# Kernel optimization log

Hardware: AMD Instinct MI355X
Metric: run time of the kernel (lower is better)

## Reference

```python
import jax, jax.numpy as jnp
import numpy as np

BATCH, N_FEATURES, D_MODEL = 8192, 8192, 1024


def setup_inputs() -> dict:
    key = jax.random.key(0)
    kx, kw = jax.random.split(key)
    # x: sparse feature activations in the original (COO); dense uniform here.
    x = jax.random.uniform(kx, (BATCH, N_FEATURES), dtype=jnp.float32)
    # Xavier-normal init for W_tr [n_features, d_model].
    std = float(np.sqrt(2.0 / (N_FEATURES + D_MODEL)))
    W_tr = jax.random.normal(kw, (N_FEATURES, D_MODEL), dtype=jnp.float32) * std
    bias = jnp.zeros((N_FEATURES,), dtype=jnp.float32)
    return {"x": x, "W_tr": W_tr, "bias": bias}


def reference(x, W_tr, bias):
    # h = x @ W_tr              : [B, n_features] @ [n_features, d_model] -> [B, d_model]
    # out = relu(h @ W_tr.T + b): [B, d_model] @ [d_model, n_features] -> [B, n_features]
    h = jnp.einsum("bf,fd->bd", x, W_tr)
    return jax.nn.relu(jnp.einsum("bd,fd->bf", h, W_tr) + bias)
```

## Files before the change

### kernel.cpp

```cpp
#include <hip/hip_runtime.h>
#include <hip/hip_bf16.h>
#include <stdint.h>

#define BATCH  8192
#define NFEAT  8192
#define DMODEL 1024

typedef unsigned short u16;
typedef __attribute__((ext_vector_type(8))) short  short8;
typedef __attribute__((ext_vector_type(4))) float  f32x4;

__device__ __forceinline__ u16 f2b(float f) {
    uint32_t u = __float_as_uint(f);
    u += 0x7fffu + ((u >> 16) & 1u);
    return (u16)(u >> 16);
}

__device__ __forceinline__ void gld16(const u16* g, void* l) {
    __builtin_amdgcn_global_load_lds(
        (const __attribute__((address_space(1))) void*)(uintptr_t)g,
        (__attribute__((address_space(3))) void*)(uint32_t)(uintptr_t)l,
        16, 0, 0);
}


__global__ void cvt_x_kernel(const float* __restrict__ x, u16* __restrict__ xb) {
    int i = blockIdx.x * blockDim.x + threadIdx.x;
    const float4* xv = (const float4*)x;
    float4 a = xv[2 * i];
    float4 b = xv[2 * i + 1];
    union { u16 u[8]; uint4 v; } o;
    o.u[0] = f2b(a.x); o.u[1] = f2b(a.y); o.u[2] = f2b(a.z); o.u[3] = f2b(a.w);
    o.u[4] = f2b(b.x); o.u[5] = f2b(b.y); o.u[6] = f2b(b.z); o.u[7] = f2b(b.w);
    ((uint4*)xb)[i] = o.v;
}

__global__ void cvt_w_kernel(const float* __restrict__ W,
                             u16* __restrict__ wb, u16* __restrict__ wt) {
    __shared__ u16 tile[64][65];
    const int f0 = blockIdx.x * 64;
    const int d0 = blockIdx.y * 64;
    const int t  = threadIdx.x;
#pragma unroll
    for (int rep = 0; rep < 16; ++rep) {
        int idx = rep * 256 + t;
        int r = idx >> 6, c = idx & 63;
        float v = W[(size_t)(f0 + r) * DMODEL + d0 + c];
        u16 u = f2b(v);
        tile[r][c] = u;
        wb[(size_t)(f0 + r) * DMODEL + d0 + c] = u;
    }
    __syncthreads();
#pragma unroll
    for (int rep = 0; rep < 16; ++rep) {
        int idx = rep * 256 + t;
        int r = idx >> 6, c = idx & 63;
        wt[(size_t)(d0 + r) * NFEAT + f0 + c] = tile[c][r];
    }
}

#define SYNC_IN()  do { __builtin_amdgcn_s_barrier(); \
                        asm volatile("s_waitcnt lgkmcnt(0)" ::: "memory"); } while (0)
#define SYNC_OUT() do { __builtin_amdgcn_s_setprio(0); __builtin_amdgcn_s_barrier(); } while (0)

__global__ __launch_bounds__(512, 2)
void gemm1_8phase(const u16* __restrict__ A, const u16* __restrict__ B,
                  u16* __restrict__ H, int N, int K) {
    const int NT = K >> 6;
    __shared__ __align__(1024) char lds[131072];
    const int BOFF = 98304;

    const int tid  = threadIdx.x;
    const int lane = tid & 63;
    const int wave = tid >> 6;
    const int wm   = wave >> 2;
    const int wn   = wave & 3;

    const int nwg = gridDim.x;
    const int swz = (blockIdx.x & 7) * (nwg >> 3) + (blockIdx.x >> 3);
    const int ntn = N >> 7;
    const int tm0 = (swz / ntn) << 8;
    const int tn0 = (swz % ntn) << 7;

    const int srl = lane >> 2;
    const int sch = (lane & 3) ^ (((lane >> 5) & 1) << 1);
    const int scol  = (wave & 1) * 32 + sch * 8;
    const int srow0 = (wave >> 1) * 16 + srl;

    const u16* pa[2][2];
    pa[0][0] = A + (size_t)(tm0 + srow0)            * K + scol;
    pa[0][1] = A + (size_t)(tm0 + srow0 + 64)       * K + scol;
    pa[1][0] = A + (size_t)(tm0 + 128 + srow0)      * K + scol;
    pa[1][1] = A + (size_t)(tm0 + 128 + srow0 + 64) * K + scol;
    const u16* pb[2];
    pb[0] = B + (size_t)(tn0 + srow0)      * K + scol;
    pb[1] = B + (size_t)(tn0 + srow0 + 64) * K + scol;

    auto STAGE_A = [&](int tau, int half) {
        if (tau < NT) {
            char* d = lds + (tau % 3) * 32768 + half * 16384 + wave * 1024;
            gld16(pa[half][0] + (size_t)tau * 64, d);
            gld16(pa[half][1] + (size_t)tau * 64, d + 8192);
        }
    };
    auto STAGE_B = [&](int tau) {
        if (tau < NT) {
            char* d = lds + BOFF + (tau & 1) * 16384 + wave * 1024;
            gld16(pb[0] + (size_t)tau * 64, d);
            gld16(pb[1] + (size_t)tau * 64, d + 8192);
        }
    };

    const int l15 = lane & 15, lhi = lane >> 4;
    const int pch = lhi ^ (((lane >> 3) & 1) << 1);
    const int lof = l15 * 64 + pch * 16;

    short8 a[4][2];
    short8 b[2][2];
    f32x4  acc[8][2] = {};

    const char* Ab;
    const char* Bb;
    auto LDA_ = [&](int mh) {
#pragma unroll
        for (int fm = 0; fm < 4; ++fm)
#pragma unroll
            for (int ks = 0; ks < 2; ++ks)
                a[fm][ks] = *(const short8*)(Ab + ((mh * 4 + fm) * 2 + ks) * 1024);
    };
    auto LDB_ = [&](int nh) {
#pragma unroll
        for (int ks = 0; ks < 2; ++ks)
            b[nh][ks] = *(const short8*)(Bb + (nh * 2 + ks) * 1024);
    };
    auto MMA_ = [&](int mh, int nh) {
#pragma unroll
        for (int ks = 0; ks < 2; ++ks)
#pragma unroll
            for (int fm = 0; fm < 4; ++fm)
                acc[mh * 4 + fm][nh] = __builtin_amdgcn_mfma_f32_16x16x32_bf16(
                    a[fm][ks], b[nh][ks], acc[mh * 4 + fm][nh], 0, 0, 0);
    };

    STAGE_A(0, 0); STAGE_A(0, 1); STAGE_B(0);
    STAGE_A(1, 0); STAGE_A(1, 1); STAGE_B(1);
    asm volatile("s_waitcnt vmcnt(6)" ::: "memory");
    __builtin_amdgcn_s_barrier();

    for (int t = 0; t < NT; ++t) {
        Ab = lds + (t % 3) * 32768 + wm * 16384 + lof;
        Bb = lds + BOFF + (t & 1) * 16384 + wn * 4096 + lof;

        LDA_(0); LDB_(0);
        STAGE_A(t + 2, 0);
        SYNC_IN();
        __builtin_amdgcn_s_setprio(1);
        MMA_(0, 0);
        SYNC_OUT();

        LDB_(1);
        STAGE_A(t + 2, 1);
        SYNC_IN();
        __builtin_amdgcn_s_setprio(1);
        MMA_(0, 1);
        SYNC_OUT();

        LDA_(1);
        STAGE_B(t + 2);
        SYNC_IN();
        __builtin_amdgcn_s_setprio(1);
        MMA_(1, 1);
        SYNC_OUT();

        __builtin_amdgcn_s_barrier();
        __builtin_amdgcn_s_setprio(1);
        MMA_(1, 0);
        __builtin_amdgcn_s_setprio(0);
        if (t < NT - 2)       asm volatile("s_waitcnt vmcnt(6)" ::: "memory");
        else if (t == NT - 2) asm volatile("s_waitcnt vmcnt(0)" ::: "memory");
        __builtin_amdgcn_s_barrier();
    }

    u16* lu = (u16*)lds;
#pragma unroll
    for (int fm = 0; fm < 8; ++fm)
#pragma unroll
        for (int nh = 0; nh < 2; ++nh) {
            const int col  = wn * 32 + nh * 16 + l15;
            const int row0 = wm * 128 + fm * 16 + lhi * 4;
#pragma unroll
            for (int r = 0; r < 4; ++r)
                lu[(row0 + r) * 128 + col] = f2b(acc[fm][nh][r]);
        }
    __syncthreads();
    const uint4* ls = (const uint4*)lds;
#pragma unroll
    for (int s = 0; s < 8; ++s) {
        int i = s * 512 + tid;
        int row = i >> 4;
        int col = (i & 15) * 8;
        *(uint4*)(H + (size_t)(tm0 + row) * N + (tn0 + col)) = ls[i];
    }
}

__global__ __launch_bounds__(512, 2)
void gemm2_8phase(const u16* __restrict__ A, const u16* __restrict__ B,
                  float* __restrict__ O, const float* __restrict__ bias,
                  int N, int K) {
    const int NT = K >> 6;
    __shared__ __align__(1024) char lds[163840];
    const int BOFF = 98304;

    const int tid  = threadIdx.x;
    const int lane = tid & 63;
    const int wave = tid >> 6;
    const int wm   = wave >> 2;
    const int wn   = wave & 3;

    const int nwg = gridDim.x;
    const int swz = (blockIdx.x & 7) * (nwg >> 3) + (blockIdx.x >> 3);
    const int ntn = N >> 8;
    const int tm0 = (swz / ntn) << 8;
    const int tn0 = (swz % ntn) << 8;

    const int srl = lane >> 2;
    const int sch = (lane & 3) ^ (((lane >> 5) & 1) << 1);
    const int scol  = (wave & 1) * 32 + sch * 8;
    const int srow0 = (wave >> 1) * 16 + srl;

    const u16* pa[2][2];
    const u16* pb[2][2];
    pa[0][0] = A + (size_t)(tm0 + srow0)       * K + scol;
    pa[0][1] = A + (size_t)(tm0 + srow0 + 64)  * K + scol;
    pa[1][0] = A + (size_t)(tm0 + 128 + srow0)      * K + scol;
    pa[1][1] = A + (size_t)(tm0 + 128 + srow0 + 64) * K + scol;
    pb[0][0] = B + (size_t)(tn0 + srow0)       * K + scol;
    pb[0][1] = B + (size_t)(tn0 + srow0 + 64)  * K + scol;
    pb[1][0] = B + (size_t)(tn0 + 128 + srow0)      * K + scol;
    pb[1][1] = B + (size_t)(tn0 + 128 + srow0 + 64) * K + scol;

    auto STAGE_A = [&](int tau, int half) {
        if (tau < NT) {
            char* d = lds + (tau % 3) * 32768 + half * 16384 + wave * 1024;
            gld16(pa[half][0] + (size_t)tau * 64, d);
            gld16(pa[half][1] + (size_t)tau * 64, d + 8192);
        }
    };
    auto STAGE_B = [&](int tau, int half) {
        if (tau < NT) {
            char* d = lds + BOFF + (tau & 1) * 32768 + half * 16384 + wave * 1024;
            gld16(pb[half][0] + (size_t)tau * 64, d);
            gld16(pb[half][1] + (size_t)tau * 64, d + 8192);
        }
    };

    const int l15 = lane & 15, lhi = lane >> 4;
    const int pch = lhi ^ (((lane >> 3) & 1) << 1);
    const int lof = l15 * 64 + pch * 16;

    short8 a[4][2];
    short8 b[4][2];
    f32x4  acc[8][4] = {};

    const char* Ab;
    const char* Bb;
    auto LDA_ = [&](int mh) {
#pragma unroll
        for (int fm = 0; fm < 4; ++fm)
#pragma unroll
            for (int ks = 0; ks < 2; ++ks)
                a[fm][ks] = *(const short8*)(Ab + ((mh * 4 + fm) * 2 + ks) * 1024);
    };
    auto LDB_ = [&](int nh) {
#pragma unroll
        for (int fn = 0; fn < 2; ++fn)
#pragma unroll
            for (int ks = 0; ks < 2; ++ks)
                b[nh * 2 + fn][ks] = *(const short8*)(Bb + (((wn & 1) * 4 + nh * 2 + fn) * 2 + ks) * 1024);
    };
    auto MMA_ = [&](int mh, int nh) {
#pragma unroll
        for (int ks = 0; ks < 2; ++ks)
#pragma unroll
            for (int fm = 0; fm < 4; ++fm)
#pragma unroll
                for (int fn = 0; fn < 2; ++fn)
                    acc[mh * 4 + fm][nh * 2 + fn] = __builtin_amdgcn_mfma_f32_16x16x32_bf16(
                        a[fm][ks], b[nh * 2 + fn][ks], acc[mh * 4 + fm][nh * 2 + fn], 0, 0, 0);
    };

    STAGE_A(0, 0); STAGE_A(0, 1); STAGE_B(0, 0); STAGE_B(0, 1);
    STAGE_A(1, 0); STAGE_A(1, 1); STAGE_B(1, 0); STAGE_B(1, 1);
    asm volatile("s_waitcnt vmcnt(8)" ::: "memory");
    __builtin_amdgcn_s_barrier();

    for (int t = 0; t < NT; ++t) {
        Ab = lds + (t % 3) * 32768 + wm * 16384 + lof;
        Bb = lds + BOFF + (t & 1) * 32768 + (wn >> 1) * 16384 + lof;

        LDA_(0); LDB_(0);
        STAGE_A(t + 2, 0);
        asm volatile("s_waitcnt lgkmcnt(8)" ::: "memory");
        SYNC_IN();
        __builtin_amdgcn_s_setprio(1);
        MMA_(0, 0);
        SYNC_OUT();

        LDB_(1);
        STAGE_A(t + 2, 1);
        SYNC_IN();
        __builtin_amdgcn_s_setprio(1);
        MMA_(0, 1);
        SYNC_OUT();

        LDA_(1);
        STAGE_B(t + 2, 0);
        SYNC_IN();
        __builtin_amdgcn_s_setprio(1);
        MMA_(1, 1);
        SYNC_OUT();

        STAGE_B(t + 2, 1);
        __builtin_amdgcn_s_barrier();
        asm volatile("s_waitcnt lgkmcnt(0)" ::: "memory");
        __builtin_amdgcn_s_setprio(1);
        MMA_(1, 0);
        __builtin_amdgcn_s_setprio(0);
        if (t < NT - 2)       asm volatile("s_waitcnt vmcnt(8)" ::: "memory");
        else if (t == NT - 2) asm volatile("s_waitcnt vmcnt(0)" ::: "memory");
        __builtin_amdgcn_s_barrier();
    }

    const int orow = tm0 + wm * 128;
    const int ocol = tn0 + wn * 64;
    float bv[4];
#pragma unroll
    for (int fn = 0; fn < 4; ++fn) bv[fn] = bias[ocol + fn * 16 + l15];
#pragma unroll
    for (int fm = 0; fm < 8; ++fm) {
        const int row0 = orow + fm * 16 + lhi * 4;
#pragma unroll
        for (int fn = 0; fn < 4; ++fn) {
            const int col = ocol + fn * 16 + l15;
#pragma unroll
            for (int r = 0; r < 4; ++r) {
                float v = acc[fm][fn][r] + bv[fn];
                O[(size_t)(row0 + r) * N + col] = v > 0.f ? v : 0.f;
            }
        }
    }
}


extern "C" void kernel_launch(void* const* d_in, const int* in_sizes, int n_in,
                              void* d_out, int out_size, void* d_ws, size_t ws_size,
                              hipStream_t stream) {
    const float* x    = (const float*)d_in[0];
    const float* W    = (const float*)d_in[1];
    const float* bias = (const float*)d_in[2];
    float* out = (float*)d_out;

    char* ws = (char*)d_ws;
    u16* xb = (u16*)ws;
    u16* wt = (u16*)(ws + 134217728);
    u16* wb = (u16*)(ws + 134217728 + 16777216);
    u16* hb = (u16*)(ws + 134217728 + 2 * 16777216);

    cvt_x_kernel<<<(BATCH * NFEAT / 8) / 256, 256, 0, stream>>>(x, xb);
    cvt_w_kernel<<<dim3(NFEAT / 64, DMODEL / 64), 256, 0, stream>>>(W, wb, wt);

    gemm1_8phase<<<dim3((BATCH / 256) * (DMODEL / 128)), 512, 0, stream>>>(
        xb, wt, hb, DMODEL, NFEAT);

    gemm2_8phase<<<dim3((BATCH / 256) * (NFEAT / 256)), 512, 0, stream>>>(
        hb, wb, out, bias, NFEAT, DMODEL);
}
```

Baseline: 390.6 us.

## Stage GEMM2 epilogue through LDS for coalesced float4 stores and regroup tile swizzle

The output tile is written to shared memory in two 128-row halves and then stored to global memory with fully coalesced float4 writes, replacing scattered per-element stores of the 256MB fp32 output. The workgroup-to-tile mapping is also changed to group tiles into 4x8 blocks for better L2 reuse of A and B. This adds extra LDS traffic and barriers in the epilogue, and the new mapping hardcodes the tile-grid dimensions.

```diff
diff --git a/kernel.cpp b/kernel.cpp
--- a/kernel.cpp
+++ b/kernel.cpp
@@ -219,9 +219,10 @@
 
     const int nwg = gridDim.x;
     const int swz = (blockIdx.x & 7) * (nwg >> 3) + (blockIdx.x >> 3);
-    const int ntn = N >> 8;
-    const int tm0 = (swz / ntn) << 8;
-    const int tn0 = (swz % ntn) << 8;
+    const int sp  = swz >> 5;
+    const int ss  = swz & 31;
+    const int tm0 = (((sp >> 2) << 2) + (ss >> 3)) << 8;
+    const int tn0 = (((sp & 3) << 3) + (ss & 7)) << 8;
 
     const int srl = lane >> 2;
     const int sch = (lane & 3) ^ (((lane >> 5) & 1) << 1);
@@ -331,23 +332,37 @@
         __builtin_amdgcn_s_barrier();
     }
 
-    const int orow = tm0 + wm * 128;
     const int ocol = tn0 + wn * 64;
     float bv[4];
 #pragma unroll
     for (int fn = 0; fn < 4; ++fn) bv[fn] = bias[ocol + fn * 16 + l15];
-#pragma unroll
-    for (int fm = 0; fm < 8; ++fm) {
-        const int row0 = orow + fm * 16 + lhi * 4;
-#pragma unroll
-        for (int fn = 0; fn < 4; ++fn) {
-            const int col = ocol + fn * 16 + l15;
-#pragma unroll
-            for (int r = 0; r < 4; ++r) {
-                float v = acc[fm][fn][r] + bv[fn];
-                O[(size_t)(row0 + r) * N + col] = v > 0.f ? v : 0.f;
-            }
-        }
+    float* lf = (float*)lds;
+#pragma unroll
+    for (int ep = 0; ep < 2; ++ep) {
+        if (wm == ep) {
+#pragma unroll
+            for (int fm = 0; fm < 8; ++fm)
+#pragma unroll
+                for (int fn = 0; fn < 4; ++fn) {
+                    const int col  = wn * 64 + fn * 16 + l15;
+                    const int row0 = fm * 16 + lhi * 4;
+#pragma unroll
+                    for (int r = 0; r < 4; ++r) {
+                        float v = acc[fm][fn][r] + bv[fn];
+                        lf[(row0 + r) * 256 + col] = v > 0.f ? v : 0.f;
+                    }
+                }
+        }
+        __syncthreads();
+        const float4* ls = (const float4*)lds;
+#pragma unroll
+        for (int s = 0; s < 16; ++s) {
+            int i = s * 512 + tid;
+            int row = i >> 6;
+            int col = (i & 63) * 4;
+            *(float4*)(O + (size_t)(tm0 + ep * 128 + row) * N + (tn0 + col)) = ls[i];
+        }
+        if (ep == 0) __syncthreads();
     }
 }
 
```

After: 403.1 us. +3.2%, slower.

## Make second GEMM persistent with four M-tiles per block and continuous pipeline

Applied to the files above, without the earlier changes.

The second GEMM now launches 256 workgroups instead of 1024. Each workgroup keeps a fixed 256-column N tile and walks four consecutive 256-row M tiles, so its K-loop pipeline runs without a break across 64 iterations. The bias/ReLU epilogue runs and the accumulators are reset every 16 iterations inside the loop. This removes per-tile prologue and drain overhead and keeps the B tile hot in cache. The cost is that the fp32 output stores now sit inside the loop and may stall the next tile's MMA work, and the grid is exactly one wave of blocks.

```diff
diff --git a/kernel.cpp b/kernel.cpp
--- a/kernel.cpp
+++ b/kernel.cpp
@@ -204,12 +204,12 @@
 }
 
 __global__ __launch_bounds__(512, 2)
-void gemm2_8phase(const u16* __restrict__ A, const u16* __restrict__ B,
-                  float* __restrict__ O, const float* __restrict__ bias,
-                  int N, int K) {
-    const int NT = K >> 6;
+void gemm2_persist(const u16* __restrict__ A, const u16* __restrict__ B,
+                   float* __restrict__ O, const float* __restrict__ bias,
+                   int N, int K) {
     __shared__ __align__(1024) char lds[163840];
     const int BOFF = 98304;
+    const int TTOT = 64;
 
     const int tid  = threadIdx.x;
     const int lane = tid & 63;
@@ -217,40 +217,33 @@
     const int wm   = wave >> 2;
     const int wn   = wave & 3;
 
-    const int nwg = gridDim.x;
-    const int swz = (blockIdx.x & 7) * (nwg >> 3) + (blockIdx.x >> 3);
-    const int ntn = N >> 8;
-    const int tm0 = (swz / ntn) << 8;
-    const int tn0 = (swz % ntn) << 8;
+    const int bid = blockIdx.x;
+    const int xcd = bid & 7;
+    const int sub = (bid >> 3) & 3;
+    const int mg  = bid >> 5;
+    const int tn0     = ((xcd << 2) + sub) << 8;
+    const int tm_base = mg << 10;
 
     const int srl = lane >> 2;
     const int sch = (lane & 3) ^ (((lane >> 5) & 1) << 1);
     const int scol  = (wave & 1) * 32 + sch * 8;
     const int srow0 = (wave >> 1) * 16 + srl;
 
-    const u16* pa[2][2];
-    const u16* pb[2][2];
-    pa[0][0] = A + (size_t)(tm0 + srow0)       * K + scol;
-    pa[0][1] = A + (size_t)(tm0 + srow0 + 64)  * K + scol;
-    pa[1][0] = A + (size_t)(tm0 + 128 + srow0)      * K + scol;
-    pa[1][1] = A + (size_t)(tm0 + 128 + srow0 + 64) * K + scol;
-    pb[0][0] = B + (size_t)(tn0 + srow0)       * K + scol;
-    pb[0][1] = B + (size_t)(tn0 + srow0 + 64)  * K + scol;
-    pb[1][0] = B + (size_t)(tn0 + 128 + srow0)      * K + scol;
-    pb[1][1] = B + (size_t)(tn0 + 128 + srow0 + 64) * K + scol;
-
     auto STAGE_A = [&](int tau, int half) {
-        if (tau < NT) {
+        if (tau < TTOT) {
             char* d = lds + (tau % 3) * 32768 + half * 16384 + wave * 1024;
-            gld16(pa[half][0] + (size_t)tau * 64, d);
-            gld16(pa[half][1] + (size_t)tau * 64, d + 8192);
+            const int rb = tm_base + ((tau >> 4) << 8) + half * 128 + srow0;
+            const u16* p = A + (size_t)rb * K + ((tau & 15) << 6) + scol;
+            gld16(p, d);
+            gld16(p + (size_t)64 * K, d + 8192);
         }
     };
     auto STAGE_B = [&](int tau, int half) {
-        if (tau < NT) {
+        if (tau < TTOT) {
             char* d = lds + BOFF + (tau & 1) * 32768 + half * 16384 + wave * 1024;
-            gld16(pb[half][0] + (size_t)tau * 64, d);
-            gld16(pb[half][1] + (size_t)tau * 64, d + 8192);
+            const u16* p = B + (size_t)(tn0 + half * 128 + srow0) * K + ((tau & 15) << 6) + scol;
+            gld16(p, d);
+            gld16(p + (size_t)64 * K, d + 8192);
         }
     };
 
@@ -288,18 +281,23 @@
                     acc[mh * 4 + fm][nh * 2 + fn] = __builtin_amdgcn_mfma_f32_16x16x32_bf16(
                         a[fm][ks], b[nh * 2 + fn][ks], acc[mh * 4 + fm][nh * 2 + fn], 0, 0, 0);
     };
+
+    const int ocol = tn0 + wn * 64;
+    float bv[4];
+#pragma unroll
+    for (int fn = 0; fn < 4; ++fn) bv[fn] = bias[ocol + fn * 16 + l15];
 
     STAGE_A(0, 0); STAGE_A(0, 1); STAGE_B(0, 0); STAGE_B(0, 1);
     STAGE_A(1, 0); STAGE_A(1, 1); STAGE_B(1, 0); STAGE_B(1, 1);
     asm volatile("s_waitcnt vmcnt(8)" ::: "memory");
     __builtin_amdgcn_s_barrier();
 
-    for (int t = 0; t < NT; ++t) {
-        Ab = lds + (t % 3) * 32768 + wm * 16384 + lof;
-        Bb = lds + BOFF + (t & 1) * 32768 + (wn >> 1) * 16384 + lof;
+    for (int tt = 0; tt < TTOT; ++tt) {
+        Ab = lds + (tt % 3) * 32768 + wm * 16384 + lof;
+        Bb = lds + BOFF + (tt & 1) * 32768 + (wn >> 1) * 16384 + lof;
 
         LDA_(0); LDB_(0);
-        STAGE_A(t + 2, 0);
+        STAGE_A(tt + 2, 0);
         asm volatile("s_waitcnt lgkmcnt(8)" ::: "memory");
         SYNC_IN();
         __builtin_amdgcn_s_setprio(1);
@@ -307,45 +305,44 @@
         SYNC_OUT();
 
         LDB_(1);
-        STAGE_A(t + 2, 1);
+        STAGE_A(tt + 2, 1);
         SYNC_IN();
         __builtin_amdgcn_s_setprio(1);
         MMA_(0, 1);
         SYNC_OUT();
 
         LDA_(1);
-        STAGE_B(t + 2, 0);
+        STAGE_B(tt + 2, 0);
         SYNC_IN();
         __builtin_amdgcn_s_setprio(1);
         MMA_(1, 1);
         SYNC_OUT();
 
-        STAGE_B(t + 2, 1);
+        STAGE_B(tt + 2, 1);
         __builtin_amdgcn_s_barrier();
         asm volatile("s_waitcnt lgkmcnt(0)" ::: "memory");
         __builtin_amdgcn_s_setprio(1);
         MMA_(1, 0);
         __builtin_amdgcn_s_setprio(0);
-        if (t < NT - 2)       asm volatile("s_waitcnt vmcnt(8)" ::: "memory");
-        else if (t == NT - 2) asm volatile("s_waitcnt vmcnt(0)" ::: "memory");
+        if (tt < TTOT - 2)       asm volatile("s_waitcnt vmcnt(8)" ::: "memory");
+        else if (tt == TTOT - 2) asm volatile("s_waitcnt vmcnt(0)" ::: "memory");
         __builtin_amdgcn_s_barrier();
-    }
-
-    const int orow = tm0 + wm * 128;
-    const int ocol = tn0 + wn * 64;
-    float bv[4];
-#pragma unroll
-    for (int fn = 0; fn < 4; ++fn) bv[fn] = bias[ocol + fn * 16 + l15];
-#pragma unroll
-    for (int fm = 0; fm < 8; ++fm) {
-        const int row0 = orow + fm * 16 + lhi * 4;
-#pragma unroll
-        for (int fn = 0; fn < 4; ++fn) {
-            const int col = ocol + fn * 16 + l15;
-#pragma unroll
-            for (int r = 0; r < 4; ++r) {
-                float v = acc[fm][fn][r] + bv[fn];
-                O[(size_t)(row0 + r) * N + col] = v > 0.f ? v : 0.f;
+
+        if ((tt & 15) == 15) {
+            const int orow = tm_base + ((tt >> 4) << 8) + wm * 128;
+#pragma unroll
+            for (int fm = 0; fm < 8; ++fm) {
+                const int row0 = orow + fm * 16 + lhi * 4;
+#pragma unroll
+                for (int fn = 0; fn < 4; ++fn) {
+                    const int col = ocol + fn * 16 + l15;
+#pragma unroll
+                    for (int r = 0; r < 4; ++r) {
+                        float v = acc[fm][fn][r] + bv[fn];
+                        O[(size_t)(row0 + r) * N + col] = v > 0.f ? v : 0.f;
+                        acc[fm][fn][r] = 0.f;
+                    }
+                }
             }
         }
     }
@@ -372,6 +369,6 @@
     gemm1_8phase<<<dim3((BATCH / 256) * (DMODEL / 128)), 512, 0, stream>>>(
         xb, wt, hb, DMODEL, NFEAT);
 
-    gemm2_8phase<<<dim3((BATCH / 256) * (NFEAT / 256)), 512, 0, stream>>>(
+    gemm2_persist<<<dim3(256), 512, 0, stream>>>(
         hb, wb, out, bias, NFEAT, DMODEL);
 }
```

Result: no change. 393.7 us (+0.8%).
